# Kernel optimization log

Hardware: AMD Instinct MI355X
Metric: run time of the kernel (lower is better)

## Reference

```python
import jax, jax.numpy as jnp
import numpy as np

NUM_FIELDS = 64
# itertools.combinations(range(n), 2) order == row-major upper-triangle (k=1)
_IU, _JU = np.triu_indices(NUM_FIELDS, k=1)
_IU = jnp.asarray(_IU)
_JU = jnp.asarray(_JU)


def setup_inputs() -> dict:
    key = jax.random.key(0)
    inputs = jax.random.normal(key, (16384, NUM_FIELDS, 32), dtype=jnp.float32)
    return {"inputs": inputs}


def reference(inputs) -> jnp.ndarray:
    # Gram matrix of field embeddings per sample: [B, F, F]
    gram = jnp.einsum("bfd,bgd->bfg", inputs, inputs)
    # Upper-triangle (i<j) pairs, same order as itertools.combinations: [B, F*(F-1)/2]
    return gram[:, _IU, _JU]
```

## Files before the change

### kernel.cpp

```cpp
#include <hip/hip_runtime.h>

#define NF 64
#define ND 32
#define NPAIR 2016

typedef __attribute__((ext_vector_type(8))) short bf16x8;
typedef __attribute__((ext_vector_type(4))) float f32x4;

__global__ __launch_bounds__(256, 4) void ip_gram_mfma(
    const float* __restrict__ in, float* __restrict__ out) {

    const int t = threadIdx.x;
    const int w = t >> 6;
    const int l = t & 63;
    const int s = blockIdx.x * 4 + w;

    const float* src = in + (size_t)s * (NF * ND);
    const int q = l >> 4;
    const int m = l & 15;

    bf16x8 fhi[4], flo[4];
    #pragma unroll
    for (int r = 0; r < 4; ++r) {
        const float* p = src + (r * 16 + m) * ND + (q << 3);
        float4 u0 = *(const float4*)p;
        float4 u1 = *(const float4*)(p + 4);
        float xv[8] = {u0.x, u0.y, u0.z, u0.w, u1.x, u1.y, u1.z, u1.w};
        #pragma unroll
        for (int e = 0; e < 8; ++e) {
            unsigned xb = __builtin_bit_cast(unsigned, xv[e]);
            fhi[r][e] = (short)(xb >> 16);
            float hf = __builtin_bit_cast(float, xb & 0xFFFF0000u);
            float lf = xv[e] - hf;
            flo[r][e] = (short)(__builtin_bit_cast(unsigned, lf) >> 16);
        }
    }

    float* dst = out + (size_t)s * NPAIR;
    #pragma unroll
    for (int ti = 0; ti < 4; ++ti) {
        #pragma unroll
        for (int tj = ti; tj < 4; ++tj) {
            f32x4 c = {0.f, 0.f, 0.f, 0.f};
            c = __builtin_amdgcn_mfma_f32_16x16x32_bf16(fhi[ti], fhi[tj], c, 0, 0, 0);
            c = __builtin_amdgcn_mfma_f32_16x16x32_bf16(fhi[ti], flo[tj], c, 0, 0, 0);
            c = __builtin_amdgcn_mfma_f32_16x16x32_bf16(flo[ti], fhi[tj], c, 0, 0, 0);
            int j = tj * 16 + m;
            #pragma unroll
            for (int r = 0; r < 4; ++r) {
                int i = ti * 16 + (q << 2) + r;
                if (ti < tj || j > i) {
                    int p = ((i * (127 - i)) >> 1) + j - i - 1;
                    dst[p] = c[r];
                }
            }
        }
    }
}

extern "C" void kernel_launch(void* const* d_in, const int* in_sizes, int n_in,
                              void* d_out, int out_size, void* d_ws, size_t ws_size,
                              hipStream_t stream) {
    const float* in = (const float*)d_in[0];
    float* out = (float*)d_out;
    const int nsamples = in_sizes[0] / (NF * ND);
    ip_gram_mfma<<<nsamples / 4, 256, 0, stream>>>(in, out);
}
```

Baseline: 252.5 us.

## Stage Gram outputs in LDS for coalesced stores and prefetch next sample

Each wave now processes four samples in sequence. The next sample's input loads are issued before the current sample's MFMA work so they overlap with compute. The scattered per-element global stores of the upper triangle are replaced by writes into a per-wave LDS buffer, followed by contiguous float4 stores of the packed 2016-element row. This targets the uncoalesced output writes and exposed load latency. In exchange it uses 32KB of LDS per block and launches a quarter as many blocks, which reduces parallelism per CU.

New measurement: 243.4 us. 1.04x faster.

```diff
diff --git a/kernel.cpp b/kernel.cpp
--- a/kernel.cpp
+++ b/kernel.cpp
@@ -3,6 +3,8 @@
 #define NF 64
 #define ND 32
 #define NPAIR 2016
+#define WPB 4
+#define SPW 4
 
 typedef __attribute__((ext_vector_type(8))) short bf16x8;
 typedef __attribute__((ext_vector_type(4))) float f32x4;
@@ -10,49 +12,78 @@
 __global__ __launch_bounds__(256, 4) void ip_gram_mfma(
     const float* __restrict__ in, float* __restrict__ out) {
 
+    __shared__ float gbuf[WPB][2048];
+
     const int t = threadIdx.x;
     const int w = t >> 6;
     const int l = t & 63;
-    const int s = blockIdx.x * 4 + w;
-
-    const float* src = in + (size_t)s * (NF * ND);
     const int q = l >> 4;
     const int m = l & 15;
 
-    bf16x8 fhi[4], flo[4];
+    float* g = gbuf[w];
+    const int sbase = blockIdx.x * (WPB * SPW) + w;
+
+    float4 raw[8];
+
+    auto issue_loads = [&](int s) {
+        const float* src = in + (size_t)s * (NF * ND);
+        #pragma unroll
+        for (int r = 0; r < 4; ++r) {
+            const float* p = src + (r * 16 + m) * ND + (q << 3);
+            raw[2 * r]     = *(const float4*)p;
+            raw[2 * r + 1] = *(const float4*)(p + 4);
+        }
+    };
+
+    issue_loads(sbase);
+
     #pragma unroll
-    for (int r = 0; r < 4; ++r) {
-        const float* p = src + (r * 16 + m) * ND + (q << 3);
-        float4 u0 = *(const float4*)p;
-        float4 u1 = *(const float4*)(p + 4);
-        float xv[8] = {u0.x, u0.y, u0.z, u0.w, u1.x, u1.y, u1.z, u1.w};
+    for (int it = 0; it < SPW; ++it) {
+        bf16x8 fhi[4], flo[4];
         #pragma unroll
-        for (int e = 0; e < 8; ++e) {
-            unsigned xb = __builtin_bit_cast(unsigned, xv[e]);
-            fhi[r][e] = (short)(xb >> 16);
-            float hf = __builtin_bit_cast(float, xb & 0xFFFF0000u);
-            float lf = xv[e] - hf;
-            flo[r][e] = (short)(__builtin_bit_cast(unsigned, lf) >> 16);
+        for (int r = 0; r < 4; ++r) {
+            float xv[8];
+            *(float4*)&xv[0] = raw[2 * r];
+            *(float4*)&xv[4] = raw[2 * r + 1];
+            #pragma unroll
+            for (int e = 0; e < 8; ++e) {
+                unsigned xb = __builtin_bit_cast(unsigned, xv[e]);
+                fhi[r][e] = (short)(xb >> 16);
+                float hf = __builtin_bit_cast(float, xb & 0xFFFF0000u);
+                float lf = xv[e] - hf;
+                flo[r][e] = (short)(__builtin_bit_cast(unsigned, lf) >> 16);
+            }
         }
-    }
 
-    float* dst = out + (size_t)s * NPAIR;
-    #pragma unroll
-    for (int ti = 0; ti < 4; ++ti) {
+        if (it + 1 < SPW) issue_loads(sbase + (it + 1) * WPB);
+
         #pragma unroll
-        for (int tj = ti; tj < 4; ++tj) {
-            f32x4 c = {0.f, 0.f, 0.f, 0.f};
-            c = __builtin_amdgcn_mfma_f32_16x16x32_bf16(fhi[ti], fhi[tj], c, 0, 0, 0);
-            c = __builtin_amdgcn_mfma_f32_16x16x32_bf16(fhi[ti], flo[tj], c, 0, 0, 0);
-            c = __builtin_amdgcn_mfma_f32_16x16x32_bf16(flo[ti], fhi[tj], c, 0, 0, 0);
-            int j = tj * 16 + m;
+        for (int ti = 0; ti < 4; ++ti) {
             #pragma unroll
-            for (int r = 0; r < 4; ++r) {
-                int i = ti * 16 + (q << 2) + r;
-                if (ti < tj || j > i) {
-                    int p = ((i * (127 - i)) >> 1) + j - i - 1;
-                    dst[p] = c[r];
+            for (int tj = ti; tj < 4; ++tj) {
+                f32x4 c = {0.f, 0.f, 0.f, 0.f};
+                c = __builtin_amdgcn_mfma_f32_16x16x32_bf16(fhi[ti], fhi[tj], c, 0, 0, 0);
+                c = __builtin_amdgcn_mfma_f32_16x16x32_bf16(fhi[ti], flo[tj], c, 0, 0, 0);
+                c = __builtin_amdgcn_mfma_f32_16x16x32_bf16(flo[ti], fhi[tj], c, 0, 0, 0);
+                int j = tj * 16 + m;
+                #pragma unroll
+                for (int r = 0; r < 4; ++r) {
+                    int i = ti * 16 + (q << 2) + r;
+                    if (ti < tj || j > i) {
+                        int p = ((i * (127 - i)) >> 1) + j - i - 1;
+                        g[p] = c[r];
+                    }
                 }
+            }
+        }
+
+        float* dst = out + (size_t)(sbase + it * WPB) * NPAIR;
+        #pragma unroll
+        for (int k = 0; k < 8; ++k) {
+            int idx4 = (k << 6) + l;
+            if (idx4 < 504) {
+                float4 v = *(const float4*)(g + (idx4 << 2));
+                *(float4*)(dst + (idx4 << 2)) = v;
             }
         }
     }
@@ -64,5 +95,5 @@
     const float* in = (const float*)d_in[0];
     float* out = (float*)d_out;
     const int nsamples = in_sizes[0] / (NF * ND);
-    ip_gram_mfma<<<nsamples / 4, 256, 0, stream>>>(in, out);
+    ip_gram_mfma<<<nsamples / (WPB * SPW), 256, 0, stream>>>(in, out);
 }
```
